# Kernel tuning notes

Hardware: AMD Instinct MI355X
Metric: run time of the kernel (lower is better)

The kernel has to match this reference:

```python
import jax, jax.numpy as jnp
import numpy as np

INPUT, HIDDEN, OUT = 256, 128, 256
B, T = 64, 2048


def _uniform(key, shape, scale):
    return jax.random.uniform(key, shape, jnp.float32, -scale, scale)


def setup_inputs() -> dict:
    key = jax.random.key(0)
    ks = jax.random.split(key, 12)
    s = 1.0 / np.sqrt(HIDDEN)  # PyTorch LSTM/Linear init range
    G = 4 * HIDDEN
    return {
        "x": jax.random.normal(ks[0], (B, T, INPUT), jnp.float32),
        "w_ih_f": _uniform(ks[1], (G, INPUT), s),
        "w_hh_f": _uniform(ks[2], (G, HIDDEN), s),
        "b_ih_f": _uniform(ks[3], (G,), s),
        "b_hh_f": _uniform(ks[4], (G,), s),
        "w_ih_b": _uniform(ks[5], (G, INPUT), s),
        "w_hh_b": _uniform(ks[6], (G, HIDDEN), s),
        "b_ih_b": _uniform(ks[7], (G,), s),
        "b_hh_b": _uniform(ks[8], (G,), s),
        "mixer_w": _uniform(ks[9], (OUT, 2 * HIDDEN), 1.0 / np.sqrt(2 * HIDDEN)),
        "mixer_b": _uniform(ks[10], (OUT,), 1.0 / np.sqrt(2 * HIDDEN)),
    }


def _lstm_dir(x, w_ih, w_hh, b_ih, b_hh, reverse):
    # x: [B,T,D]; PyTorch gate order: i, f, g, o
    h_dim = w_hh.shape[1]
    b, t, _ = x.shape
    # Precompute input projection for all timesteps (one big GEMM).
    xp = jnp.einsum('btd,gd->btg', x, w_ih) + b_ih + b_hh  # [B,T,4H]
    xp = jnp.swapaxes(xp, 0, 1)  # [T,B,4H]
    if reverse:
        xp = xp[::-1]

    def step(carry, gx):
        h, c = carry
        gates = gx + h @ w_hh.T  # [B,4H]
        i, f, g, o = jnp.split(gates, 4, axis=-1)
        c = jax.nn.sigmoid(f) * c + jax.nn.sigmoid(i) * jnp.tanh(g)
        h = jax.nn.sigmoid(o) * jnp.tanh(c)
        return (h, c), h

    h0 = jnp.zeros((b, h_dim), x.dtype)
    _, hs = jax.lax.scan(step, (h0, h0), xp)  # hs: [T,B,H]
    if reverse:
        hs = hs[::-1]
    return jnp.swapaxes(hs, 0, 1)  # [B,T,H]


def reference(x, w_ih_f, w_hh_f, b_ih_f, b_hh_f,
              w_ih_b, w_hh_b, b_ih_b, b_hh_b, mixer_w, mixer_b):
    h_fwd = _lstm_dir(x, w_ih_f, w_hh_f, b_ih_f, b_hh_f, reverse=False)
    h_bwd = _lstm_dir(x, w_ih_b, w_hh_b, b_ih_b, b_hh_b, reverse=True)
    hs = jnp.concatenate([h_fwd, h_bwd], axis=-1)  # [B,T,2H]
    return hs @ mixer_w.T + mixer_b  # [B,T,OUT]
```

## Files before the change

### kernel.cpp

```cpp
#include <hip/hip_runtime.h>
#include <hip/hip_bf16.h>

#define B_   64
#define T_   2048
#define IN_  256
#define H_   128
#define G_   512
#define M_   (B_ * T_)

typedef _Float16 half2v __attribute__((ext_vector_type(2)));
typedef __bf16 bf16x8 __attribute__((ext_vector_type(8)));
typedef float f32x4 __attribute__((ext_vector_type(4)));
typedef unsigned short u16x8 __attribute__((ext_vector_type(8)));

#define L2E_  1.442695041f

__device__ __forceinline__ float dot2f(half2v a, half2v b, float c) {
    return __builtin_amdgcn_fdot2(a, b, c, false);
}
__device__ __forceinline__ half2v mk2(float a, float b) {
    half2v h; h.x = (_Float16)a; h.y = (_Float16)b; return h;
}
__device__ __forceinline__ unsigned short f2bf(float f) {
    unsigned u = __float_as_uint(f);
    return (unsigned short)((u + 0x7fffu + ((u >> 16) & 1u)) >> 16);
}
__device__ __forceinline__ float dpp_xor1(float x) {
    int i = __float_as_int(x);
    return __int_as_float(__builtin_amdgcn_update_dpp(i, i, 0xB1, 0xF, 0xF, true));
}
__device__ __forceinline__ float dpp_xor2(float x) {
    int i = __float_as_int(x);
    return __int_as_float(__builtin_amdgcn_update_dpp(i, i, 0x4E, 0xF, 0xF, true));
}
__device__ __forceinline__ float sigp(float x) {
    return __builtin_amdgcn_rcpf(1.f + __builtin_amdgcn_exp2f(-L2E_ * x));
}
__device__ __forceinline__ float tanhp(float x) {
    return fmaf(2.f, __builtin_amdgcn_rcpf(1.f + __builtin_amdgcn_exp2f(-2.f * L2E_ * x)), -1.f);
}

__global__ __launch_bounds__(256) void gemm_in_mfma(
    const float* __restrict__ x,
    const float* __restrict__ w_f, const float* __restrict__ w_b,
    const float* __restrict__ bi_f, const float* __restrict__ bh_f,
    const float* __restrict__ bi_b, const float* __restrict__ bh_b,
    __hip_bfloat16* __restrict__ xp)
{
    const int nt  = blockIdx.x;
    const int m0  = blockIdx.y * 64;
    const int dir = nt >> 3;
    const int q0  = (nt & 7) * 16;
    const float* __restrict__ w  = dir ? w_b  : w_f;
    const float* __restrict__ bi = dir ? bi_b : bi_f;
    const float* __restrict__ bh = dir ? bh_b : bh_f;

    __shared__ alignas(16) unsigned short Asm[64 * 64];
    __shared__ alignas(16) unsigned short Bsm[64 * 64];
    __shared__ float bias_s[64];

    const int tid = threadIdx.x;
    const int wv  = tid >> 6;
    const int ln  = tid & 63;
    const int wr  = (wv >> 1) * 32;
    const int wc  = (wv & 1) * 32;
    const int l15 = ln & 15;
    const int l4  = ln >> 4;

#define STAGE_A(c2, k0) { int row = (c2) >> 3, kc = (c2) & 7; \
    const float4* sp = reinterpret_cast<const float4*>(x + (size_t)(m0 + row) * 256 + (k0) + kc * 8); \
    float4 fa = sp[0], fb = sp[1]; \
    u16x8 pk; pk[0]=f2bf(fa.x); pk[1]=f2bf(fa.y); pk[2]=f2bf(fa.z); pk[3]=f2bf(fa.w); \
    pk[4]=f2bf(fb.x); pk[5]=f2bf(fb.y); pk[6]=f2bf(fb.z); pk[7]=f2bf(fb.w); \
    *reinterpret_cast<u16x8*>(reinterpret_cast<char*>(Asm) + row * 128 + ((kc * 16) ^ ((row & 7) << 4))) = pk; }

#define STAGE_B(c2, k0) { int row = (c2) >> 3, kc = (c2) & 7; \
    int nglob = (row & 3) * 128 + q0 + (row >> 2); \
    const float4* sp = reinterpret_cast<const float4*>(w + (size_t)nglob * 256 + (k0) + kc * 8); \
    float4 fa = sp[0], fb = sp[1]; \
    u16x8 pk; pk[0]=f2bf(fa.x); pk[1]=f2bf(fa.y); pk[2]=f2bf(fa.z); pk[3]=f2bf(fa.w); \
    pk[4]=f2bf(fb.x); pk[5]=f2bf(fb.y); pk[6]=f2bf(fb.z); pk[7]=f2bf(fb.w); \
    *reinterpret_cast<u16x8*>(reinterpret_cast<char*>(Bsm) + row * 128 + ((kc * 16) ^ ((row & 7) << 4))) = pk; }

#define FRAG(BASE, rowe, kb) \
    __builtin_bit_cast(bf16x8, *reinterpret_cast<const uint4*>( \
        reinterpret_cast<const char*>(BASE) + (rowe) * 128 + ((kb) ^ (((rowe) & 7) << 4))))

    STAGE_A(tid, 0)  STAGE_A(tid + 256, 0)
    STAGE_B(tid, 0)  STAGE_B(tid + 256, 0)
    if (tid < 64) {
        int n = (tid & 3) * 128 + q0 + (tid >> 2);
        bias_s[tid] = bi[n] + bh[n];
    }
    __syncthreads();

    const float bv0 = bias_s[wc + l15];
    const float bv1 = bias_s[wc + 16 + l15];
    f32x4 acc00 = {bv0, bv0, bv0, bv0};
    f32x4 acc01 = {bv1, bv1, bv1, bv1};
    f32x4 acc10 = {bv0, bv0, bv0, bv0};
    f32x4 acc11 = {bv1, bv1, bv1, bv1};

    const int ra0 = wr + l15,      ra1 = wr + 16 + l15;
    const int rb0 = wc + l15,      rb1 = wc + 16 + l15;

    for (int kst = 0; kst < 4; ++kst) {
        if (kst) {
            __syncthreads();
            STAGE_A(tid, kst * 64)  STAGE_A(tid + 256, kst * 64)
            STAGE_B(tid, kst * 64)  STAGE_B(tid + 256, kst * 64)
            __syncthreads();
        }
        #pragma unroll
        for (int ks = 0; ks < 64; ks += 32) {
            int kb = ks * 2 + (l4 << 4);
            bf16x8 a0 = FRAG(Asm, ra0, kb);
            bf16x8 a1 = FRAG(Asm, ra1, kb);
            bf16x8 b0 = FRAG(Bsm, rb0, kb);
            bf16x8 b1 = FRAG(Bsm, rb1, kb);
            acc00 = __builtin_amdgcn_mfma_f32_16x16x32_bf16(a0, b0, acc00, 0, 0, 0);
            acc01 = __builtin_amdgcn_mfma_f32_16x16x32_bf16(a0, b1, acc01, 0, 0, 0);
            acc10 = __builtin_amdgcn_mfma_f32_16x16x32_bf16(a1, b0, acc10, 0, 0, 0);
            acc11 = __builtin_amdgcn_mfma_f32_16x16x32_bf16(a1, b1, acc11, 0, 0, 0);
        }
    }
    __syncthreads();

#define DWRITE(accv, mi, ni) { int row = wr + (mi) * 16 + l4 * 4; int col = wc + (ni) * 16 + l15; \
    Asm[(row + 0) * 64 + col] = f2bf(accv[0]); Asm[(row + 1) * 64 + col] = f2bf(accv[1]); \
    Asm[(row + 2) * 64 + col] = f2bf(accv[2]); Asm[(row + 3) * 64 + col] = f2bf(accv[3]); }
    DWRITE(acc00, 0, 0) DWRITE(acc01, 0, 1) DWRITE(acc10, 1, 0) DWRITE(acc11, 1, 1)
#undef DWRITE
    __syncthreads();

    #pragma unroll
    for (int p = 0; p < 2; ++p) {
        int c2 = tid + p * 256;
        int row = c2 >> 3, ch = c2 & 7;
        uint4 v = *reinterpret_cast<const uint4*>(reinterpret_cast<const char*>(Asm) + row * 128 + ch * 16);
        *reinterpret_cast<uint4*>(xp + ((size_t)dir * M_ + m0 + row) * G_ + q0 * 4 + ch * 8) = v;
    }
#undef STAGE_A
#undef STAGE_B
}

__global__ __launch_bounds__(512, 2) void lstm_rec(
    const __hip_bfloat16* __restrict__ xp,
    const float* __restrict__ w_hh_f,
    const float* __restrict__ w_hh_b,
    __hip_bfloat16* __restrict__ hs)
{
    const int wg  = blockIdx.x;
    const int dir = wg >> 6;
    const int b   = wg & 63;
    const int tid = threadIdx.x;
    const int s   = tid & 3;
    const int Q   = tid >> 2;
    const float* __restrict__ w_hh = dir ? w_hh_b : w_hh_f;

#define DECLW(g) half2v W##g##_0,W##g##_1,W##g##_2,W##g##_3,W##g##_4,W##g##_5,W##g##_6,W##g##_7, \
    W##g##_8,W##g##_9,W##g##_10,W##g##_11,W##g##_12,W##g##_13,W##g##_14,W##g##_15
    DECLW(0); DECLW(1); DECLW(2); DECLW(3);
#undef DECLW
#define LOADW(g) { const float4* p = reinterpret_cast<const float4*>(w_hh + (size_t)((g) * H_ + Q) * H_ + s * 32); \
    float4 r0=p[0],r1=p[1],r2=p[2],r3=p[3],r4=p[4],r5=p[5],r6=p[6],r7=p[7]; \
    W##g##_0=mk2(r0.x,r0.y);  W##g##_1=mk2(r0.z,r0.w);  W##g##_2=mk2(r1.x,r1.y);  W##g##_3=mk2(r1.z,r1.w); \
    W##g##_4=mk2(r2.x,r2.y);  W##g##_5=mk2(r2.z,r2.w);  W##g##_6=mk2(r3.x,r3.y);  W##g##_7=mk2(r3.z,r3.w); \
    W##g##_8=mk2(r4.x,r4.y);  W##g##_9=mk2(r4.z,r4.w);  W##g##_10=mk2(r5.x,r5.y); W##g##_11=mk2(r5.z,r5.w); \
    W##g##_12=mk2(r6.x,r6.y); W##g##_13=mk2(r6.z,r6.w); W##g##_14=mk2(r7.x,r7.y); W##g##_15=mk2(r7.z,r7.w); }
    LOADW(0) LOADW(1) LOADW(2) LOADW(3)
#undef LOADW

    __shared__ alignas(16) _Float16 hbuf[2][H_];
    if (tid < 2 * H_) (&hbuf[0][0])[tid] = (_Float16)0.f;
    float c = 0.f;
    __syncthreads();

    const unsigned short* __restrict__ xb =
        reinterpret_cast<const unsigned short*>(xp) + ((size_t)(dir * B_ + b)) * T_ * G_;
    __hip_bfloat16* __restrict__ ho =
        hs + (size_t)b * T_ * (2 * H_) + dir * H_ + Q;

    int t = dir ? (T_ - 1) : 0;
    const int dt = dir ? -1 : 1;

#define XPLD(sp) (*reinterpret_cast<const uint2*>(xb + (size_t)(dir ? (T_ - 1 - (sp)) : (sp)) * G_ + Q * 4))
    uint2 cur0 = XPLD(0), cur1 = XPLD(1), cur2 = XPLD(2), cur3 = XPLD(3);

#define DOT1(hw, k) { half2v hh = __builtin_bit_cast(half2v, hw); \
    p0 = dot2f(W0_##k, hh, p0); p1 = dot2f(W1_##k, hh, p1); \
    p2 = dot2f(W2_##k, hh, p2); p3 = dot2f(W3_##k, hh, p3); }

#define STEP(par, CUR) { \
    const _Float16* hp = hbuf[par]; \
    uint4 u0 = *reinterpret_cast<const uint4*>(hp + s * 32); \
    uint4 u1 = *reinterpret_cast<const uint4*>(hp + s * 32 + 8); \
    uint4 u2 = *reinterpret_cast<const uint4*>(hp + s * 32 + 16); \
    uint4 u3 = *reinterpret_cast<const uint4*>(hp + s * 32 + 24); \
    float p0 = 0.f, p1 = 0.f, p2 = 0.f, p3 = 0.f; \
    DOT1(u0.x, 0)  DOT1(u0.y, 1)  DOT1(u0.z, 2)  DOT1(u0.w, 3) \
    DOT1(u1.x, 4)  DOT1(u1.y, 5)  DOT1(u1.z, 6)  DOT1(u1.w, 7) \
    DOT1(u2.x, 8)  DOT1(u2.y, 9)  DOT1(u2.z, 10) DOT1(u2.w, 11) \
    DOT1(u3.x, 12) DOT1(u3.y, 13) DOT1(u3.z, 14) DOT1(u3.w, 15) \
    p0 += dpp_xor1(p0); p0 += dpp_xor2(p0); \
    p1 += dpp_xor1(p1); p1 += dpp_xor2(p1); \
    p2 += dpp_xor1(p2); p2 += dpp_xor2(p2); \
    p3 += dpp_xor1(p3); p3 += dpp_xor2(p3); \
    float xi = __uint_as_float(CUR.x << 16); \
    float xf = __uint_as_float(CUR.x & 0xffff0000u); \
    float xg = __uint_as_float(CUR.y << 16); \
    float xo = __uint_as_float(CUR.y & 0xffff0000u); \
    float si = sigp(p0 + xi), sf = sigp(p1 + xf); \
    float tg = tanhp(p2 + xg), so = sigp(p3 + xo); \
    c = fmaf(sf, c, si * tg); \
    float h = so * tanhp(c); \
    if (s == 0) { \
        hbuf[(par) ^ 1][Q] = (_Float16)h; \
        ho[(size_t)t * (2 * H_)] = __float2bfloat16(h); \
    } \
    asm volatile("s_waitcnt lgkmcnt(0)" ::: "memory"); \
    __builtin_amdgcn_s_barrier(); \
    t += dt; }

    for (int blk = 0; blk < T_ / 4; ++blk) {
        int base = blk * 4 + 4;
        int s0 = base     > T_ - 1 ? T_ - 1 : base;
        int s1 = base + 1 > T_ - 1 ? T_ - 1 : base + 1;
        int s2 = base + 2 > T_ - 1 ? T_ - 1 : base + 2;
        int s3 = base + 3 > T_ - 1 ? T_ - 1 : base + 3;
        uint2 nxt0 = XPLD(s0), nxt1 = XPLD(s1), nxt2 = XPLD(s2), nxt3 = XPLD(s3);

        STEP(0, cur0)
        STEP(1, cur1)
        STEP(0, cur2)
        STEP(1, cur3)

        cur0 = nxt0; cur1 = nxt1; cur2 = nxt2; cur3 = nxt3;
    }
#undef STEP
#undef DOT1
#undef XPLD
}

__global__ __launch_bounds__(256) void mixer_mfma(
    const __hip_bfloat16* __restrict__ hs,
    const float* __restrict__ mw,
    const float* __restrict__ mb,
    float* __restrict__ out)
{
    const int n0 = blockIdx.x * 64;
    const int m0 = blockIdx.y * 64;

    __shared__ alignas(16) unsigned short Asm[64 * 64];
    __shared__ alignas(16) unsigned short Bsm[64 * 64];
    __shared__ alignas(16) float Dlds[64 * 64];
    __shared__ float bias_s[64];

    const int tid = threadIdx.x;
    const int wv  = tid >> 6;
    const int ln  = tid & 63;
    const int wr  = (wv >> 1) * 32;
    const int wc  = (wv & 1) * 32;
    const int l15 = ln & 15;
    const int l4  = ln >> 4;

#define STAGE_A3(c2, k0) { int row = (c2) >> 3, kc = (c2) & 7; \
    uint4 v = *reinterpret_cast<const uint4*>(hs + (size_t)(m0 + row) * 256 + (k0) + kc * 8); \
    *reinterpret_cast<uint4*>(reinterpret_cast<char*>(Asm) + row * 128 + ((kc * 16) ^ ((row & 7) << 4))) = v; }
#define STAGE_B3(c2, k0) { int row = (c2) >> 3, kc = (c2) & 7; \
    const float4* sp = reinterpret_cast<const float4*>(mw + (size_t)(n0 + row) * 256 + (k0) + kc * 8); \
    float4 fa = sp[0], fb = sp[1]; \
    u16x8 pk; pk[0]=f2bf(fa.x); pk[1]=f2bf(fa.y); pk[2]=f2bf(fa.z); pk[3]=f2bf(fa.w); \
    pk[4]=f2bf(fb.x); pk[5]=f2bf(fb.y); pk[6]=f2bf(fb.z); pk[7]=f2bf(fb.w); \
    *reinterpret_cast<u16x8*>(reinterpret_cast<char*>(Bsm) + row * 128 + ((kc * 16) ^ ((row & 7) << 4))) = pk; }

    STAGE_A3(tid, 0)  STAGE_A3(tid + 256, 0)
    STAGE_B3(tid, 0)  STAGE_B3(tid + 256, 0)
    if (tid < 64) bias_s[tid] = mb[n0 + tid];
    __syncthreads();

    const float bv0 = bias_s[wc + l15];
    const float bv1 = bias_s[wc + 16 + l15];
    f32x4 acc00 = {bv0, bv0, bv0, bv0};
    f32x4 acc01 = {bv1, bv1, bv1, bv1};
    f32x4 acc10 = {bv0, bv0, bv0, bv0};
    f32x4 acc11 = {bv1, bv1, bv1, bv1};

    const int ra0 = wr + l15,      ra1 = wr + 16 + l15;
    const int rb0 = wc + l15,      rb1 = wc + 16 + l15;

    for (int kst = 0; kst < 4; ++kst) {
        if (kst) {
            __syncthreads();
            STAGE_A3(tid, kst * 64)  STAGE_A3(tid + 256, kst * 64)
            STAGE_B3(tid, kst * 64)  STAGE_B3(tid + 256, kst * 64)
            __syncthreads();
        }
        #pragma unroll
        for (int ks = 0; ks < 64; ks += 32) {
            int kb = ks * 2 + (l4 << 4);
            bf16x8 a0 = FRAG(Asm, ra0, kb);
            bf16x8 a1 = FRAG(Asm, ra1, kb);
            bf16x8 b0 = FRAG(Bsm, rb0, kb);
            bf16x8 b1 = FRAG(Bsm, rb1, kb);
            acc00 = __builtin_amdgcn_mfma_f32_16x16x32_bf16(a0, b0, acc00, 0, 0, 0);
            acc01 = __builtin_amdgcn_mfma_f32_16x16x32_bf16(a0, b1, acc01, 0, 0, 0);
            acc10 = __builtin_amdgcn_mfma_f32_16x16x32_bf16(a1, b0, acc10, 0, 0, 0);
            acc11 = __builtin_amdgcn_mfma_f32_16x16x32_bf16(a1, b1, acc11, 0, 0, 0);
        }
    }
    __syncthreads();

#define DWRITE3(accv, mi, ni) { int row = wr + (mi) * 16 + l4 * 4; int col = wc + (ni) * 16 + l15; \
    Dlds[(row + 0) * 64 + col] = accv[0]; Dlds[(row + 1) * 64 + col] = accv[1]; \
    Dlds[(row + 2) * 64 + col] = accv[2]; Dlds[(row + 3) * 64 + col] = accv[3]; }
    DWRITE3(acc00, 0, 0) DWRITE3(acc01, 0, 1) DWRITE3(acc10, 1, 0) DWRITE3(acc11, 1, 1)
#undef DWRITE3
    __syncthreads();

    #pragma unroll
    for (int p = 0; p < 4; ++p) {
        int c2 = tid + p * 256;
        int row = c2 >> 4, ch = c2 & 15;
        float4 v = *reinterpret_cast<const float4*>(Dlds + row * 64 + ch * 4);
        *reinterpret_cast<float4*>(out + (size_t)(m0 + row) * 256 + n0 + ch * 4) = v;
    }
#undef STAGE_A3
#undef STAGE_B3
#undef FRAG
}

extern "C" void kernel_launch(void* const* d_in, const int* in_sizes, int n_in,
                              void* d_out, int out_size, void* d_ws, size_t ws_size,
                              hipStream_t stream) {
    const float* x       = (const float*)d_in[0];
    const float* w_ih_f  = (const float*)d_in[1];
    const float* w_hh_f  = (const float*)d_in[2];
    const float* b_ih_f  = (const float*)d_in[3];
    const float* b_hh_f  = (const float*)d_in[4];
    const float* w_ih_b  = (const float*)d_in[5];
    const float* w_hh_b  = (const float*)d_in[6];
    const float* b_ih_b  = (const float*)d_in[7];
    const float* b_hh_b  = (const float*)d_in[8];
    const float* mixer_w = (const float*)d_in[9];
    const float* mixer_b = (const float*)d_in[10];
    float* out = (float*)d_out;

    const size_t xp_bytes = (size_t)2 * M_ * G_ * sizeof(__hip_bfloat16);
    const size_t hs_bytes = (size_t)M_ * 2 * H_ * sizeof(__hip_bfloat16);
    if (ws_size < xp_bytes + hs_bytes) return;

    __hip_bfloat16* xp = (__hip_bfloat16*)d_ws;
    __hip_bfloat16* hs = (__hip_bfloat16*)((char*)d_ws + xp_bytes);

    gemm_in_mfma<<<dim3(16, M_ / 64), 256, 0, stream>>>(
        x, w_ih_f, w_ih_b, b_ih_f, b_hh_f, b_ih_b, b_hh_b, xp);
    lstm_rec<<<128, 512, 0, stream>>>(xp, w_hh_f, w_hh_b, hs);
    mixer_mfma<<<dim3(4, M_ / 64), 256, 0, stream>>>(
        hs, mixer_w, mixer_b, out);
}
```

Before: 1.526 ms.

## Split LSTM recurrence work by gate per lane instead of by K-slice

Each of the four lanes per hidden unit now computes the full 128-long dot product for one gate, where before each lane computed a quarter of K for all four gates. This removes the cross-lane DPP reduction of partial sums and evaluates a single activation per lane, with the other three gate values gathered by DPP exchanges. The xp load becomes a single bf16 per lane. In exchange, every lane reads the whole h vector from LDS (16 uint4 loads) each step, and the serial dot chain per lane is longer, so per-step latency could go up.

```diff
diff --git a/kernel.cpp b/kernel.cpp
--- a/kernel.cpp
+++ b/kernel.cpp
@@ -32,9 +32,6 @@
 __device__ __forceinline__ float dpp_xor2(float x) {
     int i = __float_as_int(x);
     return __int_as_float(__builtin_amdgcn_update_dpp(i, i, 0x4E, 0xF, 0xF, true));
-}
-__device__ __forceinline__ float sigp(float x) {
-    return __builtin_amdgcn_rcpf(1.f + __builtin_amdgcn_exp2f(-L2E_ * x));
 }
 __device__ __forceinline__ float tanhp(float x) {
     return fmaf(2.f, __builtin_amdgcn_rcpf(1.f + __builtin_amdgcn_exp2f(-2.f * L2E_ * x)), -1.f);
@@ -154,22 +151,20 @@
     const int dir = wg >> 6;
     const int b   = wg & 63;
     const int tid = threadIdx.x;
-    const int s   = tid & 3;
+    const int g   = tid & 3;
     const int Q   = tid >> 2;
     const float* __restrict__ w_hh = dir ? w_hh_b : w_hh_f;
-
-#define DECLW(g) half2v W##g##_0,W##g##_1,W##g##_2,W##g##_3,W##g##_4,W##g##_5,W##g##_6,W##g##_7, \
-    W##g##_8,W##g##_9,W##g##_10,W##g##_11,W##g##_12,W##g##_13,W##g##_14,W##g##_15
-    DECLW(0); DECLW(1); DECLW(2); DECLW(3);
-#undef DECLW
-#define LOADW(g) { const float4* p = reinterpret_cast<const float4*>(w_hh + (size_t)((g) * H_ + Q) * H_ + s * 32); \
-    float4 r0=p[0],r1=p[1],r2=p[2],r3=p[3],r4=p[4],r5=p[5],r6=p[6],r7=p[7]; \
-    W##g##_0=mk2(r0.x,r0.y);  W##g##_1=mk2(r0.z,r0.w);  W##g##_2=mk2(r1.x,r1.y);  W##g##_3=mk2(r1.z,r1.w); \
-    W##g##_4=mk2(r2.x,r2.y);  W##g##_5=mk2(r2.z,r2.w);  W##g##_6=mk2(r3.x,r3.y);  W##g##_7=mk2(r3.z,r3.w); \
-    W##g##_8=mk2(r4.x,r4.y);  W##g##_9=mk2(r4.z,r4.w);  W##g##_10=mk2(r5.x,r5.y); W##g##_11=mk2(r5.z,r5.w); \
-    W##g##_12=mk2(r6.x,r6.y); W##g##_13=mk2(r6.z,r6.w); W##g##_14=mk2(r7.x,r7.y); W##g##_15=mk2(r7.z,r7.w); }
-    LOADW(0) LOADW(1) LOADW(2) LOADW(3)
-#undef LOADW
+    const float* __restrict__ wrow = w_hh + (size_t)(g * H_ + Q) * H_;
+
+#define LWC(c) half2v W##c##_0,W##c##_1,W##c##_2,W##c##_3,W##c##_4,W##c##_5,W##c##_6,W##c##_7; { \
+    const float4* p = reinterpret_cast<const float4*>(wrow + (c) * 16); \
+    float4 r0 = p[0], r1 = p[1], r2 = p[2], r3 = p[3]; \
+    W##c##_0 = mk2(r0.x, r0.y); W##c##_1 = mk2(r0.z, r0.w); \
+    W##c##_2 = mk2(r1.x, r1.y); W##c##_3 = mk2(r1.z, r1.w); \
+    W##c##_4 = mk2(r2.x, r2.y); W##c##_5 = mk2(r2.z, r2.w); \
+    W##c##_6 = mk2(r3.x, r3.y); W##c##_7 = mk2(r3.z, r3.w); }
+    LWC(0) LWC(1) LWC(2) LWC(3) LWC(4) LWC(5) LWC(6) LWC(7)
+#undef LWC
 
     __shared__ alignas(16) _Float16 hbuf[2][H_];
     if (tid < 2 * H_) (&hbuf[0][0])[tid] = (_Float16)0.f;
@@ -183,38 +178,45 @@
 
     int t = dir ? (T_ - 1) : 0;
     const int dt = dir ? -1 : 1;
-
-#define XPLD(sp) (*reinterpret_cast<const uint2*>(xb + (size_t)(dir ? (T_ - 1 - (sp)) : (sp)) * G_ + Q * 4))
-    uint2 cur0 = XPLD(0), cur1 = XPLD(1), cur2 = XPLD(2), cur3 = XPLD(3);
-
-#define DOT1(hw, k) { half2v hh = __builtin_bit_cast(half2v, hw); \
-    p0 = dot2f(W0_##k, hh, p0); p1 = dot2f(W1_##k, hh, p1); \
-    p2 = dot2f(W2_##k, hh, p2); p3 = dot2f(W3_##k, hh, p3); }
+    const float kk = (g == 2) ? (-2.f * L2E_) : (-L2E_);
+
+#define XPLD(sp) ((unsigned int)xb[(size_t)(dir ? (T_ - 1 - (sp)) : (sp)) * G_ + tid])
+    unsigned int cur0 = XPLD(0), cur1 = XPLD(1), cur2 = XPLD(2), cur3 = XPLD(3);
+
+#define DOTC(c, HA, HB, P) { \
+    P = dot2f(W##c##_0, __builtin_bit_cast(half2v, HA.x), P); \
+    P = dot2f(W##c##_1, __builtin_bit_cast(half2v, HA.y), P); \
+    P = dot2f(W##c##_2, __builtin_bit_cast(half2v, HA.z), P); \
+    P = dot2f(W##c##_3, __builtin_bit_cast(half2v, HA.w), P); \
+    P = dot2f(W##c##_4, __builtin_bit_cast(half2v, HB.x), P); \
+    P = dot2f(W##c##_5, __builtin_bit_cast(half2v, HB.y), P); \
+    P = dot2f(W##c##_6, __builtin_bit_cast(half2v, HB.z), P); \
+    P = dot2f(W##c##_7, __builtin_bit_cast(half2v, HB.w), P); }
 
 #define STEP(par, CUR) { \
-    const _Float16* hp = hbuf[par]; \
-    uint4 u0 = *reinterpret_cast<const uint4*>(hp + s * 32); \
-    uint4 u1 = *reinterpret_cast<const uint4*>(hp + s * 32 + 8); \
-    uint4 u2 = *reinterpret_cast<const uint4*>(hp + s * 32 + 16); \
-    uint4 u3 = *reinterpret_cast<const uint4*>(hp + s * 32 + 24); \
-    float p0 = 0.f, p1 = 0.f, p2 = 0.f, p3 = 0.f; \
-    DOT1(u0.x, 0)  DOT1(u0.y, 1)  DOT1(u0.z, 2)  DOT1(u0.w, 3) \
-    DOT1(u1.x, 4)  DOT1(u1.y, 5)  DOT1(u1.z, 6)  DOT1(u1.w, 7) \
-    DOT1(u2.x, 8)  DOT1(u2.y, 9)  DOT1(u2.z, 10) DOT1(u2.w, 11) \
-    DOT1(u3.x, 12) DOT1(u3.y, 13) DOT1(u3.z, 14) DOT1(u3.w, 15) \
-    p0 += dpp_xor1(p0); p0 += dpp_xor2(p0); \
-    p1 += dpp_xor1(p1); p1 += dpp_xor2(p1); \
-    p2 += dpp_xor1(p2); p2 += dpp_xor2(p2); \
-    p3 += dpp_xor1(p3); p3 += dpp_xor2(p3); \
-    float xi = __uint_as_float(CUR.x << 16); \
-    float xf = __uint_as_float(CUR.x & 0xffff0000u); \
-    float xg = __uint_as_float(CUR.y << 16); \
-    float xo = __uint_as_float(CUR.y & 0xffff0000u); \
-    float si = sigp(p0 + xi), sf = sigp(p1 + xf); \
-    float tg = tanhp(p2 + xg), so = sigp(p3 + xo); \
+    const uint4* hv = reinterpret_cast<const uint4*>(hbuf[par]); \
+    uint4 h0 = hv[0],  h1 = hv[1],  h2 = hv[2],  h3 = hv[3]; \
+    uint4 h4 = hv[4],  h5 = hv[5],  h6 = hv[6],  h7 = hv[7]; \
+    uint4 h8 = hv[8],  h9 = hv[9],  h10 = hv[10], h11 = hv[11]; \
+    uint4 h12 = hv[12], h13 = hv[13], h14 = hv[14], h15 = hv[15]; \
+    float pa = __uint_as_float(CUR << 16), pb = 0.f, pc = 0.f, pd = 0.f; \
+    DOTC(0, h0,  h1,  pa)  DOTC(1, h2,  h3,  pb) \
+    DOTC(2, h4,  h5,  pc)  DOTC(3, h6,  h7,  pd) \
+    DOTC(4, h8,  h9,  pa)  DOTC(5, h10, h11, pb) \
+    DOTC(6, h12, h13, pc)  DOTC(7, h14, h15, pd) \
+    float pre = (pa + pb) + (pc + pd); \
+    float y   = __builtin_amdgcn_rcpf(1.f + __builtin_amdgcn_exp2f(kk * pre)); \
+    float act = (g == 2) ? fmaf(2.f, y, -1.f) : y; \
+    float e1 = dpp_xor1(act); \
+    float e2 = dpp_xor2(act); \
+    float e3 = dpp_xor1(e2); \
+    float si = (g==0)?act:(g==1)?e1:(g==2)?e2:e3; \
+    float sf = (g==1)?act:(g==0)?e1:(g==3)?e2:e3; \
+    float tg = (g==2)?act:(g==3)?e1:(g==0)?e2:e3; \
+    float so = (g==3)?act:(g==2)?e1:(g==1)?e2:e3; \
     c = fmaf(sf, c, si * tg); \
     float h = so * tanhp(c); \
-    if (s == 0) { \
+    if (g == 0) { \
         hbuf[(par) ^ 1][Q] = (_Float16)h; \
         ho[(size_t)t * (2 * H_)] = __float2bfloat16(h); \
     } \
@@ -228,7 +230,7 @@
         int s1 = base + 1 > T_ - 1 ? T_ - 1 : base + 1;
         int s2 = base + 2 > T_ - 1 ? T_ - 1 : base + 2;
         int s3 = base + 3 > T_ - 1 ? T_ - 1 : base + 3;
-        uint2 nxt0 = XPLD(s0), nxt1 = XPLD(s1), nxt2 = XPLD(s2), nxt3 = XPLD(s3);
+        unsigned int nxt0 = XPLD(s0), nxt1 = XPLD(s1), nxt2 = XPLD(s2), nxt3 = XPLD(s3);
 
         STEP(0, cur0)
         STEP(1, cur1)
@@ -238,7 +240,7 @@
         cur0 = nxt0; cur1 = nxt1; cur2 = nxt2; cur3 = nxt3;
     }
 #undef STEP
-#undef DOT1
+#undef DOTC
 #undef XPLD
 }
 
```

New measurement: 1.587 ms. 1.04x slower.

## Compute LSTM recurrent matvec with MFMA instead of packed fdot2

Applied to the files above, without the earlier changes.

The recurrent step's h·W_hh product now uses 16x16x32 f16 MFMA instructions. Gate rows are interleaved so each 16-row tile holds i/f/g/o for four hidden units, and the precomputed input projection is preloaded into the accumulators. This removes the per-thread fdot2 chains and DPP cross-lane reductions. In exchange, the single h vector is broadcast across the MFMA N dimension, so most of the matrix compute is redundant, and only a quarter of lanes write h.

```diff
diff --git a/kernel.cpp b/kernel.cpp
--- a/kernel.cpp
+++ b/kernel.cpp
@@ -8,30 +8,16 @@
 #define G_   512
 #define M_   (B_ * T_)
 
-typedef _Float16 half2v __attribute__((ext_vector_type(2)));
 typedef __bf16 bf16x8 __attribute__((ext_vector_type(8)));
+typedef _Float16 f16x8 __attribute__((ext_vector_type(8)));
 typedef float f32x4 __attribute__((ext_vector_type(4)));
 typedef unsigned short u16x8 __attribute__((ext_vector_type(8)));
 
 #define L2E_  1.442695041f
 
-__device__ __forceinline__ float dot2f(half2v a, half2v b, float c) {
-    return __builtin_amdgcn_fdot2(a, b, c, false);
-}
-__device__ __forceinline__ half2v mk2(float a, float b) {
-    half2v h; h.x = (_Float16)a; h.y = (_Float16)b; return h;
-}
 __device__ __forceinline__ unsigned short f2bf(float f) {
     unsigned u = __float_as_uint(f);
     return (unsigned short)((u + 0x7fffu + ((u >> 16) & 1u)) >> 16);
-}
-__device__ __forceinline__ float dpp_xor1(float x) {
-    int i = __float_as_int(x);
-    return __int_as_float(__builtin_amdgcn_update_dpp(i, i, 0xB1, 0xF, 0xF, true));
-}
-__device__ __forceinline__ float dpp_xor2(float x) {
-    int i = __float_as_int(x);
-    return __int_as_float(__builtin_amdgcn_update_dpp(i, i, 0x4E, 0xF, 0xF, true));
 }
 __device__ __forceinline__ float sigp(float x) {
     return __builtin_amdgcn_rcpf(1.f + __builtin_amdgcn_exp2f(-L2E_ * x));
@@ -154,68 +140,91 @@
     const int dir = wg >> 6;
     const int b   = wg & 63;
     const int tid = threadIdx.x;
-    const int s   = tid & 3;
-    const int Q   = tid >> 2;
+    const int wv  = tid >> 6;
+    const int l   = tid & 63;
+    const int l15 = l & 15;
+    const int l4  = l >> 4;
+    const int nsel = l15 & 3;
     const float* __restrict__ w_hh = dir ? w_hh_b : w_hh_f;
 
-#define DECLW(g) half2v W##g##_0,W##g##_1,W##g##_2,W##g##_3,W##g##_4,W##g##_5,W##g##_6,W##g##_7, \
-    W##g##_8,W##g##_9,W##g##_10,W##g##_11,W##g##_12,W##g##_13,W##g##_14,W##g##_15
-    DECLW(0); DECLW(1); DECLW(2); DECLW(3);
-#undef DECLW
-#define LOADW(g) { const float4* p = reinterpret_cast<const float4*>(w_hh + (size_t)((g) * H_ + Q) * H_ + s * 32); \
-    float4 r0=p[0],r1=p[1],r2=p[2],r3=p[3],r4=p[4],r5=p[5],r6=p[6],r7=p[7]; \
-    W##g##_0=mk2(r0.x,r0.y);  W##g##_1=mk2(r0.z,r0.w);  W##g##_2=mk2(r1.x,r1.y);  W##g##_3=mk2(r1.z,r1.w); \
-    W##g##_4=mk2(r2.x,r2.y);  W##g##_5=mk2(r2.z,r2.w);  W##g##_6=mk2(r3.x,r3.y);  W##g##_7=mk2(r3.z,r3.w); \
-    W##g##_8=mk2(r4.x,r4.y);  W##g##_9=mk2(r4.z,r4.w);  W##g##_10=mk2(r5.x,r5.y); W##g##_11=mk2(r5.z,r5.w); \
-    W##g##_12=mk2(r6.x,r6.y); W##g##_13=mk2(r6.z,r6.w); W##g##_14=mk2(r7.x,r7.y); W##g##_15=mk2(r7.z,r7.w); }
-    LOADW(0) LOADW(1) LOADW(2) LOADW(3)
-#undef LOADW
+#define LDA(nt, kt) f16x8 W##nt##_##kt; { \
+    int r = 16 * (4 * wv + (nt)) + l15; \
+    const float* p = w_hh + (size_t)((r & 3) * 128 + (r >> 2)) * 128 + 32 * (kt) + 8 * l4; \
+    float4 u0 = *reinterpret_cast<const float4*>(p); \
+    float4 u1 = *reinterpret_cast<const float4*>(p + 4); \
+    W##nt##_##kt[0] = (_Float16)u0.x; W##nt##_##kt[1] = (_Float16)u0.y; \
+    W##nt##_##kt[2] = (_Float16)u0.z; W##nt##_##kt[3] = (_Float16)u0.w; \
+    W##nt##_##kt[4] = (_Float16)u1.x; W##nt##_##kt[5] = (_Float16)u1.y; \
+    W##nt##_##kt[6] = (_Float16)u1.z; W##nt##_##kt[7] = (_Float16)u1.w; }
+    LDA(0,0) LDA(0,1) LDA(0,2) LDA(0,3)
+    LDA(1,0) LDA(1,1) LDA(1,2) LDA(1,3)
+    LDA(2,0) LDA(2,1) LDA(2,2) LDA(2,3)
+    LDA(3,0) LDA(3,1) LDA(3,2) LDA(3,3)
+#undef LDA
 
     __shared__ alignas(16) _Float16 hbuf[2][H_];
     if (tid < 2 * H_) (&hbuf[0][0])[tid] = (_Float16)0.f;
-    float c = 0.f;
     __syncthreads();
 
     const unsigned short* __restrict__ xb =
         reinterpret_cast<const unsigned short*>(xp) + ((size_t)(dir * B_ + b)) * T_ * G_;
+    const int Qsel = 16 * wv + 4 * nsel + l4;
     __hip_bfloat16* __restrict__ ho =
-        hs + (size_t)b * T_ * (2 * H_) + dir * H_ + Q;
-
+        hs + (size_t)b * T_ * (2 * H_) + dir * H_ + Qsel;
+    _Float16* const hw1 = &hbuf[1][Qsel];
+    _Float16* const hw0 = &hbuf[0][Qsel];
+    const bool writer = (l15 < 4);
+
+    float c_own = 0.f;
     int t = dir ? (T_ - 1) : 0;
     const int dt = dir ? -1 : 1;
 
-#define XPLD(sp) (*reinterpret_cast<const uint2*>(xb + (size_t)(dir ? (T_ - 1 - (sp)) : (sp)) * G_ + Q * 4))
-    uint2 cur0 = XPLD(0), cur1 = XPLD(1), cur2 = XPLD(2), cur3 = XPLD(3);
-
-#define DOT1(hw, k) { half2v hh = __builtin_bit_cast(half2v, hw); \
-    p0 = dot2f(W0_##k, hh, p0); p1 = dot2f(W1_##k, hh, p1); \
-    p2 = dot2f(W2_##k, hh, p2); p3 = dot2f(W3_##k, hh, p3); }
-
-#define STEP(par, CUR) { \
-    const _Float16* hp = hbuf[par]; \
-    uint4 u0 = *reinterpret_cast<const uint4*>(hp + s * 32); \
-    uint4 u1 = *reinterpret_cast<const uint4*>(hp + s * 32 + 8); \
-    uint4 u2 = *reinterpret_cast<const uint4*>(hp + s * 32 + 16); \
-    uint4 u3 = *reinterpret_cast<const uint4*>(hp + s * 32 + 24); \
-    float p0 = 0.f, p1 = 0.f, p2 = 0.f, p3 = 0.f; \
-    DOT1(u0.x, 0)  DOT1(u0.y, 1)  DOT1(u0.z, 2)  DOT1(u0.w, 3) \
-    DOT1(u1.x, 4)  DOT1(u1.y, 5)  DOT1(u1.z, 6)  DOT1(u1.w, 7) \
-    DOT1(u2.x, 8)  DOT1(u2.y, 9)  DOT1(u2.z, 10) DOT1(u2.w, 11) \
-    DOT1(u3.x, 12) DOT1(u3.y, 13) DOT1(u3.z, 14) DOT1(u3.w, 15) \
-    p0 += dpp_xor1(p0); p0 += dpp_xor2(p0); \
-    p1 += dpp_xor1(p1); p1 += dpp_xor2(p1); \
-    p2 += dpp_xor1(p2); p2 += dpp_xor2(p2); \
-    p3 += dpp_xor1(p3); p3 += dpp_xor2(p3); \
-    float xi = __uint_as_float(CUR.x << 16); \
-    float xf = __uint_as_float(CUR.x & 0xffff0000u); \
-    float xg = __uint_as_float(CUR.y << 16); \
-    float xo = __uint_as_float(CUR.y & 0xffff0000u); \
-    float si = sigp(p0 + xi), sf = sigp(p1 + xf); \
-    float tg = tanhp(p2 + xg), so = sigp(p3 + xo); \
-    c = fmaf(sf, c, si * tg); \
-    float h = so * tanhp(c); \
-    if (s == 0) { \
-        hbuf[(par) ^ 1][Q] = (_Float16)h; \
+    const int b0 = 16 * (4 * wv + 0) + 4 * l4;
+    const int b1 = 16 * (4 * wv + 1) + 4 * l4;
+    const int b2 = 16 * (4 * wv + 2) + 4 * l4;
+    const int b3 = 16 * (4 * wv + 3) + 4 * l4;
+
+#define XPLD(sp, off) (*reinterpret_cast<const uint2*>( \
+    xb + (size_t)(dir ? (T_ - 1 - (sp)) : (sp)) * G_ + (off)))
+
+    uint2 cA0 = XPLD(0, b0), cA1 = XPLD(0, b1), cA2 = XPLD(0, b2), cA3 = XPLD(0, b3);
+    uint2 cB0 = XPLD(1, b0), cB1 = XPLD(1, b1), cB2 = XPLD(1, b2), cB3 = XPLD(1, b3);
+    uint2 cC0 = XPLD(2, b0), cC1 = XPLD(2, b1), cC2 = XPLD(2, b2), cC3 = XPLD(2, b3);
+    uint2 cD0 = XPLD(3, b0), cD1 = XPLD(3, b1), cD2 = XPLD(3, b2), cD3 = XPLD(3, b3);
+
+#define LOF(u) __uint_as_float((u) << 16)
+#define HIF(u) __uint_as_float((u) & 0xffff0000u)
+#define MFMA16(A, B, C) __builtin_amdgcn_mfma_f32_16x16x32_f16(A, B, C, 0, 0, 0)
+
+#define STEP(par, X0, X1, X2, X3, HW) { \
+    const char* hp = reinterpret_cast<const char*>(&hbuf[par][0]); \
+    f16x8 hb0 = *reinterpret_cast<const f16x8*>(hp + l4 * 16); \
+    f16x8 hb1 = *reinterpret_cast<const f16x8*>(hp + 64 + l4 * 16); \
+    f16x8 hb2 = *reinterpret_cast<const f16x8*>(hp + 128 + l4 * 16); \
+    f16x8 hb3 = *reinterpret_cast<const f16x8*>(hp + 192 + l4 * 16); \
+    f32x4 a0, a1, a2, a3; \
+    a0[0] = LOF(X0.x); a0[1] = HIF(X0.x); a0[2] = LOF(X0.y); a0[3] = HIF(X0.y); \
+    a1[0] = LOF(X1.x); a1[1] = HIF(X1.x); a1[2] = LOF(X1.y); a1[3] = HIF(X1.y); \
+    a2[0] = LOF(X2.x); a2[1] = HIF(X2.x); a2[2] = LOF(X2.y); a2[3] = HIF(X2.y); \
+    a3[0] = LOF(X3.x); a3[1] = HIF(X3.x); a3[2] = LOF(X3.y); a3[3] = HIF(X3.y); \
+    a0 = MFMA16(W0_0, hb0, a0); a1 = MFMA16(W1_0, hb0, a1); \
+    a2 = MFMA16(W2_0, hb0, a2); a3 = MFMA16(W3_0, hb0, a3); \
+    a0 = MFMA16(W0_1, hb1, a0); a1 = MFMA16(W1_1, hb1, a1); \
+    a2 = MFMA16(W2_1, hb1, a2); a3 = MFMA16(W3_1, hb1, a3); \
+    a0 = MFMA16(W0_2, hb2, a0); a1 = MFMA16(W1_2, hb2, a1); \
+    a2 = MFMA16(W2_2, hb2, a2); a3 = MFMA16(W3_2, hb2, a3); \
+    a0 = MFMA16(W0_3, hb3, a0); a1 = MFMA16(W1_3, hb3, a1); \
+    a2 = MFMA16(W2_3, hb3, a2); a3 = MFMA16(W3_3, hb3, a3); \
+    float gi = nsel == 0 ? a0[0] : nsel == 1 ? a1[0] : nsel == 2 ? a2[0] : a3[0]; \
+    float gf = nsel == 0 ? a0[1] : nsel == 1 ? a1[1] : nsel == 2 ? a2[1] : a3[1]; \
+    float gg = nsel == 0 ? a0[2] : nsel == 1 ? a1[2] : nsel == 2 ? a2[2] : a3[2]; \
+    float go = nsel == 0 ? a0[3] : nsel == 1 ? a1[3] : nsel == 2 ? a2[3] : a3[3]; \
+    float si = sigp(gi), sf = sigp(gf); \
+    float tg = tanhp(gg), so = sigp(go); \
+    c_own = fmaf(sf, c_own, si * tg); \
+    float h = so * tanhp(c_own); \
+    if (writer) { \
+        *(HW) = (_Float16)h; \
         ho[(size_t)t * (2 * H_)] = __float2bfloat16(h); \
     } \
     asm volatile("s_waitcnt lgkmcnt(0)" ::: "memory"); \
@@ -228,17 +237,25 @@
         int s1 = base + 1 > T_ - 1 ? T_ - 1 : base + 1;
         int s2 = base + 2 > T_ - 1 ? T_ - 1 : base + 2;
         int s3 = base + 3 > T_ - 1 ? T_ - 1 : base + 3;
-        uint2 nxt0 = XPLD(s0), nxt1 = XPLD(s1), nxt2 = XPLD(s2), nxt3 = XPLD(s3);
-
-        STEP(0, cur0)
-        STEP(1, cur1)
-        STEP(0, cur2)
-        STEP(1, cur3)
-
-        cur0 = nxt0; cur1 = nxt1; cur2 = nxt2; cur3 = nxt3;
+        uint2 nA0 = XPLD(s0, b0), nA1 = XPLD(s0, b1), nA2 = XPLD(s0, b2), nA3 = XPLD(s0, b3);
+        uint2 nB0 = XPLD(s1, b0), nB1 = XPLD(s1, b1), nB2 = XPLD(s1, b2), nB3 = XPLD(s1, b3);
+        uint2 nC0 = XPLD(s2, b0), nC1 = XPLD(s2, b1), nC2 = XPLD(s2, b2), nC3 = XPLD(s2, b3);
+        uint2 nD0 = XPLD(s3, b0), nD1 = XPLD(s3, b1), nD2 = XPLD(s3, b2), nD3 = XPLD(s3, b3);
+
+        STEP(0, cA0, cA1, cA2, cA3, hw1)
+        STEP(1, cB0, cB1, cB2, cB3, hw0)
+        STEP(0, cC0, cC1, cC2, cC3, hw1)
+        STEP(1, cD0, cD1, cD2, cD3, hw0)
+
+        cA0 = nA0; cA1 = nA1; cA2 = nA2; cA3 = nA3;
+        cB0 = nB0; cB1 = nB1; cB2 = nB2; cB3 = nB3;
+        cC0 = nC0; cC1 = nC1; cC2 = nC2; cC3 = nC3;
+        cD0 = nD0; cD1 = nD1; cD2 = nD2; cD3 = nD3;
     }
 #undef STEP
-#undef DOT1
+#undef MFMA16
+#undef LOF
+#undef HIF
 #undef XPLD
 }
 
```

After: 1.915 ms. 1.25x slower.

## Split recurrent dot products over 8 lanes per unit with prepacked fp16 weights

Applied to the files above, without the earlier changes.

The recurrence kernel grows from 512 to 1024 threads, so each hidden unit's four gate dot products are spread over 8 lanes of 16 elements instead of 4 lanes of 32. An extra DPP row-half-mirror step completes the 8-lane reduction. A new pre-kernel converts w_hh to fp16 in a per-thread contiguous layout, which lets each thread load its register-resident weights with a few 16-byte loads and no conversion. The aim is to shorten the serial per-timestep dot-product chain on the critical path, at the cost of a barrier across twice as many waves and an extra small launch.

```diff
diff --git a/kernel.cpp b/kernel.cpp
--- a/kernel.cpp
+++ b/kernel.cpp
@@ -8,23 +8,23 @@
 #define G_   512
 #define M_   (B_ * T_)
 
+typedef __bf16 bf16x8 __attribute__((ext_vector_type(8)));
 typedef _Float16 half2v __attribute__((ext_vector_type(2)));
-typedef __bf16 bf16x8 __attribute__((ext_vector_type(8)));
 typedef float f32x4 __attribute__((ext_vector_type(4)));
 typedef unsigned short u16x8 __attribute__((ext_vector_type(8)));
 
 #define L2E_  1.442695041f
 
-__device__ __forceinline__ float dot2f(half2v a, half2v b, float c) {
-    return __builtin_amdgcn_fdot2(a, b, c, false);
-}
-__device__ __forceinline__ half2v mk2(float a, float b) {
-    half2v h; h.x = (_Float16)a; h.y = (_Float16)b; return h;
-}
 __device__ __forceinline__ unsigned short f2bf(float f) {
     unsigned u = __float_as_uint(f);
     return (unsigned short)((u + 0x7fffu + ((u >> 16) & 1u)) >> 16);
 }
+__device__ __forceinline__ float dot2f(half2v a, half2v b, float c) {
+    return __builtin_amdgcn_fdot2(a, b, c, false);
+}
+__device__ __forceinline__ half2v h2(unsigned int u) {
+    return __builtin_bit_cast(half2v, u);
+}
 __device__ __forceinline__ float dpp_xor1(float x) {
     int i = __float_as_int(x);
     return __int_as_float(__builtin_amdgcn_update_dpp(i, i, 0xB1, 0xF, 0xF, true));
@@ -33,11 +33,30 @@
     int i = __float_as_int(x);
     return __int_as_float(__builtin_amdgcn_update_dpp(i, i, 0x4E, 0xF, 0xF, true));
 }
+__device__ __forceinline__ float dpp_xor7(float x) {
+    int i = __float_as_int(x);
+    return __int_as_float(__builtin_amdgcn_update_dpp(i, i, 0x141, 0xF, 0xF, true));
+}
 __device__ __forceinline__ float sigp(float x) {
     return __builtin_amdgcn_rcpf(1.f + __builtin_amdgcn_exp2f(-L2E_ * x));
 }
 __device__ __forceinline__ float tanhp(float x) {
     return fmaf(2.f, __builtin_amdgcn_rcpf(1.f + __builtin_amdgcn_exp2f(-2.f * L2E_ * x)), -1.f);
+}
+
+__global__ __launch_bounds__(256) void conv_whh(
+    const float* __restrict__ wf, const float* __restrict__ wb,
+    _Float16* __restrict__ wp)
+{
+    int idx = blockIdx.x * 256 + threadIdx.x;
+    int g   = idx & 3;
+    int Qs  = (idx >> 2) & 1023;
+    int dir = idx >> 12;
+    int Q = Qs >> 3, s = Qs & 7;
+    const float* src = (dir ? wb : wf) + (size_t)(g * H_ + Q) * H_ + s * 16;
+    _Float16* dst = wp + (size_t)idx * 16;
+    #pragma unroll
+    for (int k = 0; k < 16; ++k) dst[k] = (_Float16)src[k];
 }
 
 __global__ __launch_bounds__(256) void gemm_in_mfma(
@@ -144,32 +163,26 @@
 #undef STAGE_B
 }
 
-__global__ __launch_bounds__(512, 2) void lstm_rec(
+__global__ __launch_bounds__(1024)
+__attribute__((amdgpu_waves_per_eu(4, 4)))
+void lstm_rec(
     const __hip_bfloat16* __restrict__ xp,
-    const float* __restrict__ w_hh_f,
-    const float* __restrict__ w_hh_b,
+    const _Float16* __restrict__ wp,
     __hip_bfloat16* __restrict__ hs)
 {
     const int wg  = blockIdx.x;
     const int dir = wg >> 6;
     const int b   = wg & 63;
     const int tid = threadIdx.x;
-    const int s   = tid & 3;
-    const int Q   = tid >> 2;
-    const float* __restrict__ w_hh = dir ? w_hh_b : w_hh_f;
-
-#define DECLW(g) half2v W##g##_0,W##g##_1,W##g##_2,W##g##_3,W##g##_4,W##g##_5,W##g##_6,W##g##_7, \
-    W##g##_8,W##g##_9,W##g##_10,W##g##_11,W##g##_12,W##g##_13,W##g##_14,W##g##_15
-    DECLW(0); DECLW(1); DECLW(2); DECLW(3);
-#undef DECLW
-#define LOADW(g) { const float4* p = reinterpret_cast<const float4*>(w_hh + (size_t)((g) * H_ + Q) * H_ + s * 32); \
-    float4 r0=p[0],r1=p[1],r2=p[2],r3=p[3],r4=p[4],r5=p[5],r6=p[6],r7=p[7]; \
-    W##g##_0=mk2(r0.x,r0.y);  W##g##_1=mk2(r0.z,r0.w);  W##g##_2=mk2(r1.x,r1.y);  W##g##_3=mk2(r1.z,r1.w); \
-    W##g##_4=mk2(r2.x,r2.y);  W##g##_5=mk2(r2.z,r2.w);  W##g##_6=mk2(r3.x,r3.y);  W##g##_7=mk2(r3.z,r3.w); \
-    W##g##_8=mk2(r4.x,r4.y);  W##g##_9=mk2(r4.z,r4.w);  W##g##_10=mk2(r5.x,r5.y); W##g##_11=mk2(r5.z,r5.w); \
-    W##g##_12=mk2(r6.x,r6.y); W##g##_13=mk2(r6.z,r6.w); W##g##_14=mk2(r7.x,r7.y); W##g##_15=mk2(r7.z,r7.w); }
-    LOADW(0) LOADW(1) LOADW(2) LOADW(3)
-#undef LOADW
+    const int Q   = tid >> 3;
+    const int s   = tid & 7;
+
+    const uint4* wq = reinterpret_cast<const uint4*>(
+        wp + ((size_t)dir * 1024 + tid) * 64);
+    uint4 W00 = wq[0], W01 = wq[1];
+    uint4 W10 = wq[2], W11 = wq[3];
+    uint4 W20 = wq[4], W21 = wq[5];
+    uint4 W30 = wq[6], W31 = wq[7];
 
     __shared__ alignas(16) _Float16 hbuf[2][H_];
     if (tid < 2 * H_) (&hbuf[0][0])[tid] = (_Float16)0.f;
@@ -184,28 +197,27 @@
     int t = dir ? (T_ - 1) : 0;
     const int dt = dir ? -1 : 1;
 
-#define XPLD(sp) (*reinterpret_cast<const uint2*>(xb + (size_t)(dir ? (T_ - 1 - (sp)) : (sp)) * G_ + Q * 4))
+#define XPLD(sp) (*reinterpret_cast<const uint2*>( \
+    xb + (size_t)(dir ? (T_ - 1 - (sp)) : (sp)) * G_ + Q * 4))
     uint2 cur0 = XPLD(0), cur1 = XPLD(1), cur2 = XPLD(2), cur3 = XPLD(3);
 
-#define DOT1(hw, k) { half2v hh = __builtin_bit_cast(half2v, hw); \
-    p0 = dot2f(W0_##k, hh, p0); p1 = dot2f(W1_##k, hh, p1); \
-    p2 = dot2f(W2_##k, hh, p2); p3 = dot2f(W3_##k, hh, p3); }
+#define D8(WA, WB, P) { \
+    P = dot2f(h2(WA.x), h2(u0.x), P); P = dot2f(h2(WA.y), h2(u0.y), P); \
+    P = dot2f(h2(WA.z), h2(u0.z), P); P = dot2f(h2(WA.w), h2(u0.w), P); \
+    P = dot2f(h2(WB.x), h2(u1.x), P); P = dot2f(h2(WB.y), h2(u1.y), P); \
+    P = dot2f(h2(WB.z), h2(u1.z), P); P = dot2f(h2(WB.w), h2(u1.w), P); }
 
 #define STEP(par, CUR) { \
-    const _Float16* hp = hbuf[par]; \
-    uint4 u0 = *reinterpret_cast<const uint4*>(hp + s * 32); \
-    uint4 u1 = *reinterpret_cast<const uint4*>(hp + s * 32 + 8); \
-    uint4 u2 = *reinterpret_cast<const uint4*>(hp + s * 32 + 16); \
-    uint4 u3 = *reinterpret_cast<const uint4*>(hp + s * 32 + 24); \
+    const _Float16* hp = hbuf[par] + s * 16; \
+    uint4 u0 = *reinterpret_cast<const uint4*>(hp); \
+    uint4 u1 = *reinterpret_cast<const uint4*>(hp + 8); \
     float p0 = 0.f, p1 = 0.f, p2 = 0.f, p3 = 0.f; \
-    DOT1(u0.x, 0)  DOT1(u0.y, 1)  DOT1(u0.z, 2)  DOT1(u0.w, 3) \
-    DOT1(u1.x, 4)  DOT1(u1.y, 5)  DOT1(u1.z, 6)  DOT1(u1.w, 7) \
-    DOT1(u2.x, 8)  DOT1(u2.y, 9)  DOT1(u2.z, 10) DOT1(u2.w, 11) \
-    DOT1(u3.x, 12) DOT1(u3.y, 13) DOT1(u3.z, 14) DOT1(u3.w, 15) \
-    p0 += dpp_xor1(p0); p0 += dpp_xor2(p0); \
-    p1 += dpp_xor1(p1); p1 += dpp_xor2(p1); \
-    p2 += dpp_xor1(p2); p2 += dpp_xor2(p2); \
-    p3 += dpp_xor1(p3); p3 += dpp_xor2(p3); \
+    D8(W00, W01, p0)  D8(W10, W11, p1) \
+    D8(W20, W21, p2)  D8(W30, W31, p3) \
+    p0 += dpp_xor1(p0); p0 += dpp_xor2(p0); p0 += dpp_xor7(p0); \
+    p1 += dpp_xor1(p1); p1 += dpp_xor2(p1); p1 += dpp_xor7(p1); \
+    p2 += dpp_xor1(p2); p2 += dpp_xor2(p2); p2 += dpp_xor7(p2); \
+    p3 += dpp_xor1(p3); p3 += dpp_xor2(p3); p3 += dpp_xor7(p3); \
     float xi = __uint_as_float(CUR.x << 16); \
     float xf = __uint_as_float(CUR.x & 0xffff0000u); \
     float xg = __uint_as_float(CUR.y << 16); \
@@ -238,7 +250,7 @@
         cur0 = nxt0; cur1 = nxt1; cur2 = nxt2; cur3 = nxt3;
     }
 #undef STEP
-#undef DOT1
+#undef D8
 #undef XPLD
 }
 
@@ -273,6 +285,10 @@
     u16x8 pk; pk[0]=f2bf(fa.x); pk[1]=f2bf(fa.y); pk[2]=f2bf(fa.z); pk[3]=f2bf(fa.w); \
     pk[4]=f2bf(fb.x); pk[5]=f2bf(fb.y); pk[6]=f2bf(fb.z); pk[7]=f2bf(fb.w); \
     *reinterpret_cast<u16x8*>(reinterpret_cast<char*>(Bsm) + row * 128 + ((kc * 16) ^ ((row & 7) << 4))) = pk; }
+
+#define FRAG(BASE, rowe, kb) \
+    __builtin_bit_cast(bf16x8, *reinterpret_cast<const uint4*>( \
+        reinterpret_cast<const char*>(BASE) + (rowe) * 128 + ((kb) ^ (((rowe) & 7) << 4))))
 
     STAGE_A3(tid, 0)  STAGE_A3(tid + 256, 0)
     STAGE_B3(tid, 0)  STAGE_B3(tid + 256, 0)
@@ -348,14 +364,17 @@
 
     const size_t xp_bytes = (size_t)2 * M_ * G_ * sizeof(__hip_bfloat16);
     const size_t hs_bytes = (size_t)M_ * 2 * H_ * sizeof(__hip_bfloat16);
-    if (ws_size < xp_bytes + hs_bytes) return;
+    const size_t wp_bytes = (size_t)2 * 1024 * 64 * sizeof(_Float16);
+    if (ws_size < xp_bytes + hs_bytes + wp_bytes) return;
 
     __hip_bfloat16* xp = (__hip_bfloat16*)d_ws;
     __hip_bfloat16* hs = (__hip_bfloat16*)((char*)d_ws + xp_bytes);
-
+    _Float16*       wpb = (_Float16*)((char*)d_ws + xp_bytes + hs_bytes);
+
+    conv_whh<<<32, 256, 0, stream>>>(w_hh_f, w_hh_b, wpb);
     gemm_in_mfma<<<dim3(16, M_ / 64), 256, 0, stream>>>(
         x, w_ih_f, w_ih_b, b_ih_f, b_hh_f, b_ih_b, b_hh_b, xp);
-    lstm_rec<<<128, 512, 0, stream>>>(xp, w_hh_f, w_hh_b, hs);
+    lstm_rec<<<128, 1024, 0, stream>>>(xp, wpb, hs);
     mixer_mfma<<<dim3(4, M_ / 64), 256, 0, stream>>>(
         hs, mixer_w, mixer_b, out);
 }
```

After: 1.981 ms. +29.8%, slower.
